# Kernel tuning notes

Measured on AMD Instinct MI355X. Metric: run time of the kernel, lower is better.

Reference implementation:

```python
import jax, jax.numpy as jnp
import numpy as np

B, N, F = 16, 1024, 256
HEADS, K, DOUT = 8, 512, 256
TAU = 1.0
EPS = 1e-08


def setup_inputs() -> dict:
    key = jax.random.key(0)
    k1, k2, k3, k4, k5, k6 = jax.random.split(key, 6)
    return {
        'Q': jax.random.normal(k1, (B, N, F), dtype=jnp.float32),
        'keys': jax.random.uniform(k2, (HEADS, K, F), dtype=jnp.float32),
        'conv_w': jax.random.normal(k3, (HEADS,), dtype=jnp.float32),
        'lin_w': jax.random.normal(k4, (DOUT, F), dtype=jnp.float32) * 0.05,
        'lin_b': jax.random.normal(k5, (DOUT,), dtype=jnp.float32) * 0.05,
        'mask': jax.random.randint(k6, (B, N), 0, 2, dtype=jnp.int32),
    }


def kl_reg(C):
    # C: (B, N, K)
    P = C ** 2
    cn = jnp.sum(C, axis=-2, keepdims=True) + EPS          # sum over N
    P = P / cn
    pn = jnp.sum(P, axis=-1, keepdims=True) + EPS          # sum over K
    P = P / pn
    kl = jnp.sum(P * (jnp.log(P + EPS) - jnp.log(C + EPS)))
    return 100.0 * kl


def memconv_fwd(Q, keys, conv_w, lin_w, lin_b, fmask):
    # pairwise L2 distance Q (B,N,F) vs keys (H,K,F) -> C (B,H,N,K)
    q2 = jnp.sum(Q * Q, axis=-1)                            # (B,N)
    k2 = jnp.sum(keys * keys, axis=-1)                      # (H,K)
    qk = jnp.einsum('bnf,hkf->bhnk', Q, keys)               # (B,H,N,K)
    d2 = q2[:, None, :, None] + k2[None, :, None, :] - 2.0 * qk
    C = jnp.sqrt(jnp.maximum(d2, 0.0))
    em = fmask[:, None, :, None]                            # (B,1,N,1) broadcast
    C = C * em
    # student-t kernel (gmn variant)
    C = (1.0 + C ** 2 / TAU) ** (-(0.5 * TAU + 0.5))
    C = C / jnp.sum(C, axis=-1, keepdims=True)
    C = C * em
    # conv1x1 over heads -> (B,N,K)
    C = jnp.einsum('bhnk,h->bnk', C, conv_w)
    C = jax.nn.softmax(C, axis=-1)
    C = C * fmask[:, :, None]
    kl = kl_reg(C)
    V = jnp.einsum('bnk,bnf->bkf', C, Q)                    # (B,K,F)
    out = jax.nn.leaky_relu(jnp.einsum('bkf,of->bko', V, lin_w) + lin_b, 0.01)
    return out, kl


def reference(Q, keys, conv_w, lin_w, lin_b, mask):
    fmask = mask.astype(Q.dtype)
    return memconv_fwd(Q, keys, conv_w, lin_w, lin_b, fmask)
```

## Files before the change

kernel.cpp:

```cpp
#include <hip/hip_runtime.h>
#include <math.h>

#define Bc 16
#define Nc 1024
#define Fc 256
#define Hc 8
#define Kc 512
#define DOUTc 256
#define EPSc 1e-8f

typedef short v8s __attribute__((ext_vector_type(8)));
typedef float v4f __attribute__((ext_vector_type(4)));

__device__ __forceinline__ float waveReduceSum(float v) {
    v += __shfl_xor(v, 32); v += __shfl_xor(v, 16); v += __shfl_xor(v, 8);
    v += __shfl_xor(v, 4);  v += __shfl_xor(v, 2);  v += __shfl_xor(v, 1);
    return v;
}

__device__ __forceinline__ unsigned short f2bf(float f) {
    unsigned int u = __float_as_uint(f);
    u = (u + 0x7fffu + ((u >> 16) & 1u)) >> 16;
    return (unsigned short)u;
}

__device__ __forceinline__ void lds_barrier() {
    __builtin_amdgcn_s_waitcnt(0xC07F);
    __builtin_amdgcn_s_barrier();
}

__global__ __launch_bounds__(256) void prep_all(
    const float* __restrict__ Q, const float* __restrict__ keys,
    const float* __restrict__ lin_w,
    float* __restrict__ k2g, unsigned short* __restrict__ Kp,
    unsigned short* __restrict__ Qbp, unsigned short* __restrict__ Wp,
    float* __restrict__ cn, float* __restrict__ klout) {
    __shared__ unsigned short T2[32][66];
    const int bx = blockIdx.x;
    const int tid = threadIdx.x;
    if (bx < 1024) {
        int row = bx * 4 + (tid >> 6);
        int l = tid & 63;
        float4 v = *(const float4*)(keys + (size_t)row * Fc + l * 4);
        float s = v.x * v.x + v.y * v.y + v.z * v.z + v.w * v.w;
        s = waveReduceSum(s);
        if (l == 0) k2g[row] = s;
    } else if (bx < 1536) {
        int t = (bx - 1024) * 256 + tid;
        int lane = t & 63, ci = t >> 6;
        int ct = ci & 7, ks = (ci >> 3) & 7, wv = (ci >> 6) & 3, h = ci >> 8;
        int qd = lane >> 4, li = lane & 15;
        int col = h * 512 + wv * 128 + ct * 16 + li;
        const float* src = keys + (size_t)col * Fc + ks * 32 + qd * 8;
        float4 a = *(const float4*)src;
        float4 b = *(const float4*)(src + 4);
        *(ushort4*)(Kp + (size_t)t * 8) = make_ushort4(f2bf(a.x), f2bf(a.y), f2bf(a.z), f2bf(a.w));
        *(ushort4*)(Kp + (size_t)t * 8 + 4) = make_ushort4(f2bf(b.x), f2bf(b.y), f2bf(b.z), f2bf(b.w));
    } else if (bx < 3584) {
        int i = bx - 1536;
        int n0 = (i & 31) * 32, f0 = ((i >> 5) & 3) * 64, bb = i >> 7;
        {
            int n_l = tid >> 3, f_l = (tid & 7) * 8;
            const float* src = Q + ((size_t)(bb * Nc + n0 + n_l)) * Fc + f0 + f_l;
            float4 a = *(const float4*)src;
            float4 b = *(const float4*)(src + 4);
            T2[n_l][f_l + 0] = f2bf(a.x); T2[n_l][f_l + 1] = f2bf(a.y);
            T2[n_l][f_l + 2] = f2bf(a.z); T2[n_l][f_l + 3] = f2bf(a.w);
            T2[n_l][f_l + 4] = f2bf(b.x); T2[n_l][f_l + 5] = f2bf(b.y);
            T2[n_l][f_l + 6] = f2bf(b.z); T2[n_l][f_l + 7] = f2bf(b.w);
        }
        __syncthreads();
        int c = tid >> 6, L = tid & 63;
        int qd = L >> 4, li = L & 15;
        unsigned short o[8];
#pragma unroll
        for (int j = 0; j < 8; j++) o[j] = T2[qd * 8 + j][c * 16 + li];
        size_t idx = ((((size_t)bb * 16 + (f0 >> 4) + c) * 32 + (n0 >> 5)) * 64 + L) * 8;
        *(ushort4*)(Qbp + idx) = make_ushort4(o[0], o[1], o[2], o[3]);
        *(ushort4*)(Qbp + idx + 4) = make_ushort4(o[4], o[5], o[6], o[7]);
    } else if (bx < 3616) {
        int t = (bx - 3584) * 256 + tid;
        int lane = t & 63, ci = t >> 6;
        int ot = ci >> 3, fs = ci & 7;
        int qd = lane >> 4, li = lane & 15;
        const float* src = lin_w + (size_t)(ot * 16 + li) * Fc + fs * 32 + qd * 8;
        float4 a = *(const float4*)src;
        float4 b = *(const float4*)(src + 4);
        *(ushort4*)(Wp + (size_t)t * 8) = make_ushort4(f2bf(a.x), f2bf(a.y), f2bf(a.z), f2bf(a.w));
        *(ushort4*)(Wp + (size_t)t * 8 + 4) = make_ushort4(f2bf(b.x), f2bf(b.y), f2bf(b.z), f2bf(b.w));
    } else {
        int i = (bx - 3616) * 256 + tid;
        float4 z = make_float4(0.f, 0.f, 0.f, 0.f);
        float4* d = (float4*)(cn + (size_t)i * 16);
        d[0] = z; d[1] = z; d[2] = z; d[3] = z;
        if (bx == 3616 && tid == 0) *klout = 0.f;
    }
}

__global__ __launch_bounds__(256, 2) void cmfma_kernel(
    const float* __restrict__ Q, const unsigned short* __restrict__ Kp,
    const float* __restrict__ k2g, const float* __restrict__ conv_w,
    const int* __restrict__ mask, float* __restrict__ C,
    float* __restrict__ cn, unsigned short* __restrict__ Ctp) {
    __shared__ __align__(16) char uni[36864];
    __shared__ float q2h[4][16];
    __shared__ float msh[32];
    __shared__ float redb[Hc][4][32];
    __shared__ float mslot[4][32];
    __shared__ float eslot[4][32];
    float* k2s = (float*)uni;
    short* Ash = (short*)(uni + 16384);
    short (*Tb)[36] = (short (*)[36])uni;

    const int tid = threadIdx.x;
    const int wv = tid >> 6, L = tid & 63;
    const int qd = L >> 4, li = L & 15;
    const int gr0 = blockIdx.x * 32;
    const int b = gr0 >> 10;

    {
        int s_ = wv >> 1;
        int ksbase = (wv & 1) * 4;
        const float* qrow = Q + (size_t)(gr0 + s_ * 16 + li) * Fc + qd * 8;
        float q2part = 0.f;
#pragma unroll
        for (int j = 0; j < 4; j++) {
            int ks = ksbase + j;
            float4 a = *(const float4*)(qrow + ks * 32);
            float4 bq = *(const float4*)(qrow + ks * 32 + 4);
            v8s f;
            f[0] = (short)f2bf(a.x);  f[1] = (short)f2bf(a.y);
            f[2] = (short)f2bf(a.z);  f[3] = (short)f2bf(a.w);
            f[4] = (short)f2bf(bq.x); f[5] = (short)f2bf(bq.y);
            f[6] = (short)f2bf(bq.z); f[7] = (short)f2bf(bq.w);
            *(v8s*)&Ash[(((s_ * 8 + ks) * 64) + L) * 8] = f;
            q2part += a.x * a.x + a.y * a.y + a.z * a.z + a.w * a.w +
                      bq.x * bq.x + bq.y * bq.y + bq.z * bq.z + bq.w * bq.w;
        }
        q2part += __shfl_xor(q2part, 16);
        q2part += __shfl_xor(q2part, 32);
        if (qd == 0) q2h[wv][li] = q2part;
    }
    if (tid < 32) msh[tid] = (float)mask[gr0 + tid];
    for (int i = tid; i < Hc * Kc / 4; i += 256)
        *(float4*)&k2s[i * 4] = *(const float4*)(k2g + i * 4);

    v4f D[2][8], S[2][8];
#pragma unroll
    for (int s = 0; s < 2; s++)
#pragma unroll
        for (int ct = 0; ct < 8; ct++) {
            D[s][ct] = (v4f){0.f, 0.f, 0.f, 0.f};
            S[s][ct] = (v4f){0.f, 0.f, 0.f, 0.f};
        }

    const unsigned short* kwbase = Kp + (size_t)L * 8;
    v8s Bc0[8], Bn[8];
    {
        const unsigned short* p0 = kwbase + (size_t)(wv * 64) * 512;
#pragma unroll
        for (int ct = 0; ct < 8; ct++) Bc0[ct] = *(const v8s*)(p0 + ct * 512);
    }

    lds_barrier();

    float q2r[2][4], mrow[2][4];
#pragma unroll
    for (int s = 0; s < 2; s++)
#pragma unroll
        for (int r = 0; r < 4; r++) {
            q2r[s][r] = q2h[2 * s][qd * 4 + r] + q2h[2 * s + 1][qd * 4 + r];
            mrow[s][r] = msh[s * 16 + qd * 4 + r];
        }

#define LD_A(s, kk) (*(const v8s*)&Ash[(((s) * 8 + (kk)) * 64 + L) * 8])

    v8s Ac0 = LD_A(0, 0);
    v8s Ac1 = LD_A(1, 0);

#define KSTEP(kk, CUR, NXT)                                                        \
    do {                                                                           \
        int hn = h * 8 + (kk) + 1;                                                 \
        int hh = (hn >> 3) & 7, kn = hn & 7;                                       \
        const unsigned short* pb =                                                 \
            kwbase + (size_t)(((hh * 4 + wv) * 64 + kn * 8)) * 512;                \
        _Pragma("unroll") for (int ct = 0; ct < 8; ct++)                           \
            NXT[ct] = *(const v8s*)(pb + ct * 512);                                \
        v8s An0 = LD_A(0, ((kk) + 1) & 7);                                         \
        v8s An1 = LD_A(1, ((kk) + 1) & 7);                                         \
        _Pragma("unroll") for (int ct = 0; ct < 8; ct++)                           \
            D[0][ct] = __builtin_amdgcn_mfma_f32_16x16x32_bf16(Ac0, CUR[ct],       \
                                                               D[0][ct], 0, 0, 0);\
        _Pragma("unroll") for (int ct = 0; ct < 8; ct++)                           \
            D[1][ct] = __builtin_amdgcn_mfma_f32_16x16x32_bf16(Ac1, CUR[ct],       \
                                                               D[1][ct], 0, 0, 0);\
        Ac0 = An0; Ac1 = An1;                                                      \
    } while (0)

    for (int h = 0; h < Hc; ++h) {
        KSTEP(0, Bc0, Bn); KSTEP(1, Bn, Bc0);
        KSTEP(2, Bc0, Bn); KSTEP(3, Bn, Bc0);
        KSTEP(4, Bc0, Bn); KSTEP(5, Bn, Bc0);
        KSTEP(6, Bc0, Bn); KSTEP(7, Bn, Bc0);

        float rs[2][4] = {{0.f, 0.f, 0.f, 0.f}, {0.f, 0.f, 0.f, 0.f}};
#pragma unroll
        for (int ct = 0; ct < 8; ct++) {
            float k2v = k2s[h * Kc + wv * 128 + ct * 16 + li];
#pragma unroll
            for (int s = 0; s < 2; s++)
#pragma unroll
                for (int r = 0; r < 4; r++) {
                    float d2 = fmaxf(q2r[s][r] + k2v - 2.f * D[s][ct][r], 0.f) * mrow[s][r];
                    float t = __builtin_amdgcn_rcpf(1.f + d2);
                    D[s][ct][r] = t;
                    rs[s][r] += t;
                }
        }
#pragma unroll
        for (int s = 0; s < 2; s++)
#pragma unroll
            for (int r = 0; r < 4; r++) {
                rs[s][r] += __shfl_xor(rs[s][r], 1, 16);
                rs[s][r] += __shfl_xor(rs[s][r], 2, 16);
                rs[s][r] += __shfl_xor(rs[s][r], 4, 16);
                rs[s][r] += __shfl_xor(rs[s][r], 8, 16);
            }
        if (li == 0) {
#pragma unroll
            for (int s = 0; s < 2; s++)
#pragma unroll
                for (int r = 0; r < 4; r++) redb[h][wv][s * 16 + qd * 4 + r] = rs[s][r];
        }
        lds_barrier();
        float wh = conv_w[h];
        float sc[2][4];
#pragma unroll
        for (int s = 0; s < 2; s++)
#pragma unroll
            for (int r = 0; r < 4; r++) {
                int rw = s * 16 + qd * 4 + r;
                float tot = redb[h][0][rw] + redb[h][1][rw] + redb[h][2][rw] + redb[h][3][rw];
                sc[s][r] = wh * __builtin_amdgcn_rcpf(tot);
            }
#pragma unroll
        for (int s = 0; s < 2; s++)
#pragma unroll
            for (int ct = 0; ct < 8; ct++)
#pragma unroll
                for (int r = 0; r < 4; r++) {
                    S[s][ct][r] += sc[s][r] * D[s][ct][r];
                    D[s][ct][r] = 0.f;
                }
    }
#undef KSTEP
#undef LD_A

    float mx[2][4] = {{-1e30f, -1e30f, -1e30f, -1e30f}, {-1e30f, -1e30f, -1e30f, -1e30f}};
#pragma unroll
    for (int s = 0; s < 2; s++)
#pragma unroll
        for (int ct = 0; ct < 8; ct++)
#pragma unroll
            for (int r = 0; r < 4; r++) mx[s][r] = fmaxf(mx[s][r], S[s][ct][r]);
#pragma unroll
    for (int s = 0; s < 2; s++)
#pragma unroll
        for (int r = 0; r < 4; r++) {
            mx[s][r] = fmaxf(mx[s][r], __shfl_xor(mx[s][r], 1, 16));
            mx[s][r] = fmaxf(mx[s][r], __shfl_xor(mx[s][r], 2, 16));
            mx[s][r] = fmaxf(mx[s][r], __shfl_xor(mx[s][r], 4, 16));
            mx[s][r] = fmaxf(mx[s][r], __shfl_xor(mx[s][r], 8, 16));
        }
    if (li == 0) {
#pragma unroll
        for (int s = 0; s < 2; s++)
#pragma unroll
            for (int r = 0; r < 4; r++) mslot[wv][s * 16 + qd * 4 + r] = mx[s][r];
    }
    lds_barrier();
#pragma unroll
    for (int s = 0; s < 2; s++)
#pragma unroll
        for (int r = 0; r < 4; r++) {
            int rw = s * 16 + qd * 4 + r;
            mx[s][r] = fmaxf(fmaxf(mslot[0][rw], mslot[1][rw]),
                             fmaxf(mslot[2][rw], mslot[3][rw]));
        }
    float es[2][4] = {{0.f, 0.f, 0.f, 0.f}, {0.f, 0.f, 0.f, 0.f}};
#pragma unroll
    for (int s = 0; s < 2; s++)
#pragma unroll
        for (int ct = 0; ct < 8; ct++)
#pragma unroll
            for (int r = 0; r < 4; r++) {
                float e = __expf(S[s][ct][r] - mx[s][r]);
                S[s][ct][r] = e;
                es[s][r] += e;
            }
#pragma unroll
    for (int s = 0; s < 2; s++)
#pragma unroll
        for (int r = 0; r < 4; r++) {
            es[s][r] += __shfl_xor(es[s][r], 1, 16);
            es[s][r] += __shfl_xor(es[s][r], 2, 16);
            es[s][r] += __shfl_xor(es[s][r], 4, 16);
            es[s][r] += __shfl_xor(es[s][r], 8, 16);
        }
    if (li == 0) {
#pragma unroll
        for (int s = 0; s < 2; s++)
#pragma unroll
            for (int r = 0; r < 4; r++) eslot[wv][s * 16 + qd * 4 + r] = es[s][r];
    }
    lds_barrier();
    float inv[2][4];
#pragma unroll
    for (int s = 0; s < 2; s++)
#pragma unroll
        for (int r = 0; r < 4; r++) {
            int rw = s * 16 + qd * 4 + r;
            float tot = eslot[0][rw] + eslot[1][rw] + eslot[2][rw] + eslot[3][rw];
            inv[s][r] = mrow[s][r] / tot;
        }
#pragma unroll
    for (int ct = 0; ct < 8; ct++) {
        int k = wv * 128 + ct * 16 + li;
        float colsum = 0.f;
#pragma unroll
        for (int s = 0; s < 2; s++) {
            float cv[4];
#pragma unroll
            for (int r = 0; r < 4; r++) {
                cv[r] = S[s][ct][r] * inv[s][r];
                C[(size_t)(gr0 + s * 16 + qd * 4 + r) * Kc + k] = cv[r];
                colsum += cv[r];
            }
            short4 t4;
            t4.x = (short)f2bf(cv[0]); t4.y = (short)f2bf(cv[1]);
            t4.z = (short)f2bf(cv[2]); t4.w = (short)f2bf(cv[3]);
            *(short4*)&Tb[k][s * 16 + qd * 4] = t4;
        }
        colsum += __shfl_xor(colsum, 16);
        colsum += __shfl_xor(colsum, 32);
        if (qd == 0) atomicAdd(&cn[b * Kc + k], colsum);
    }
    lds_barrier();
    {
        const int ns0 = (gr0 & 1023) >> 5;
#pragma unroll
        for (int kk = 0; kk < 2; kk++) {
            int k = tid * 2 + kk;
            int kt = k >> 4, klo = k & 15;
            size_t cbase = (((size_t)b * 32 + kt) * 32 + ns0) * 512;
#pragma unroll
            for (int q2i = 0; q2i < 4; q2i++) {
                short4 lo = *(short4*)&Tb[k][q2i * 8];
                short4 hi = *(short4*)&Tb[k][q2i * 8 + 4];
                short4* d = (short4*)(Ctp + cbase + (size_t)(q2i * 16 + klo) * 8);
                d[0] = lo; d[1] = hi;
            }
        }
    }
}

__global__ __launch_bounds__(256) void klv_kernel(
    const unsigned short* __restrict__ Ctp, const unsigned short* __restrict__ Qbp,
    unsigned short* __restrict__ Vp, const float* __restrict__ C,
    const float* __restrict__ cn, float* __restrict__ klout) {
    __shared__ short Vt[64][76];
    __shared__ float red[4];
    int tid = threadIdx.x;
    int bx = blockIdx.x;
    if (bx < 512) {
        int w = tid >> 6, L = tid & 63;
        int qd = L >> 4, li = L & 15;
        int wr = w >> 1, wc = w & 1;
        int bb = bx >> 5;
        int rem = bx & 31;
        int ktb = rem >> 2, ftb = rem & 3;
        int KT0 = ktb * 4 + wr * 2;
        int FT0 = ftb * 4 + wc * 2;
        const unsigned short* pa0 = Ctp + (((size_t)bb * 32 + KT0) * 32) * 512 + L * 8;
        const unsigned short* pa1 = pa0 + (size_t)32 * 512;
        const unsigned short* pb0 = Qbp + (((size_t)bb * 16 + FT0) * 32) * 512 + L * 8;
        const unsigned short* pb1 = pb0 + (size_t)32 * 512;
        v4f acc[2][2];
#pragma unroll
        for (int a = 0; a < 2; a++)
#pragma unroll
            for (int c = 0; c < 2; c++) acc[a][c] = (v4f){0.f, 0.f, 0.f, 0.f};

        v8s A0 = *(const v8s*)pa0, A1 = *(const v8s*)pa1;
        v8s B0 = *(const v8s*)pb0, B1 = *(const v8s*)pb1;
        for (int ns = 0; ns < 32; ns++) {
            int nsn = (ns + 1) & 31;
            v8s A0n = *(const v8s*)(pa0 + nsn * 512);
            v8s A1n = *(const v8s*)(pa1 + nsn * 512);
            v8s B0n = *(const v8s*)(pb0 + nsn * 512);
            v8s B1n = *(const v8s*)(pb1 + nsn * 512);
            acc[0][0] = __builtin_amdgcn_mfma_f32_16x16x32_bf16(A0, B0, acc[0][0], 0, 0, 0);
            acc[0][1] = __builtin_amdgcn_mfma_f32_16x16x32_bf16(A0, B1, acc[0][1], 0, 0, 0);
            acc[1][0] = __builtin_amdgcn_mfma_f32_16x16x32_bf16(A1, B0, acc[1][0], 0, 0, 0);
            acc[1][1] = __builtin_amdgcn_mfma_f32_16x16x32_bf16(A1, B1, acc[1][1], 0, 0, 0);
            A0 = A0n; A1 = A1n; B0 = B0n; B1 = B1n;
        }
#pragma unroll
        for (int a = 0; a < 2; a++)
#pragma unroll
            for (int c = 0; c < 2; c++)
#pragma unroll
                for (int r = 0; r < 4; r++)
                    Vt[(wr * 2 + a) * 16 + qd * 4 + r][(wc * 2 + c) * 16 + li] =
                        (short)f2bf(acc[a][c][r]);
        __syncthreads();
        {
            int ci = tid >> 5, s5 = tid & 31;
            int mtl = ci >> 1, fsl = ci & 1;
            size_t mt_g = (size_t)bb * 32 + ktb * 4 + mtl;
            size_t fs_g = (size_t)ftb * 2 + fsl;
#pragma unroll
            for (int half = 0; half < 2; half++) {
                int L2 = s5 + half * 32;
                int qd2 = L2 >> 4, li2 = L2 & 15;
                short4 x0 = *(short4*)&Vt[mtl * 16 + li2][fsl * 32 + qd2 * 8];
                short4 x1 = *(short4*)&Vt[mtl * 16 + li2][fsl * 32 + qd2 * 8 + 4];
                short4* d = (short4*)(Vp + ((mt_g * 8 + fs_g) * 64 + L2) * 8);
                d[0] = x0; d[1] = x1;
            }
        }
    } else {
        int bk = bx - 512;
        int w = tid >> 6, l = tid & 63;
        float kacc = 0.f;
#pragma unroll
        for (int rr = 0; rr < 4; rr++) {
            int row = bk * 16 + w * 4 + rr;
            int b = row >> 10;
            const float* cp = C + (size_t)row * Kc + l * 8;
            const float* np = cn + b * Kc + l * 8;
            float4 c0 = *(const float4*)cp;
            float4 c1 = *(const float4*)(cp + 4);
            float4 n0 = *(const float4*)np;
            float4 n1 = *(const float4*)(np + 4);
            float p[8];
            p[0] = c0.x * c0.x / (n0.x + EPSc); p[1] = c0.y * c0.y / (n0.y + EPSc);
            p[2] = c0.z * c0.z / (n0.z + EPSc); p[3] = c0.w * c0.w / (n0.w + EPSc);
            p[4] = c1.x * c1.x / (n1.x + EPSc); p[5] = c1.y * c1.y / (n1.y + EPSc);
            p[6] = c1.z * c1.z / (n1.z + EPSc); p[7] = c1.w * c1.w / (n1.w + EPSc);
            float s = p[0] + p[1] + p[2] + p[3] + p[4] + p[5] + p[6] + p[7];
            float pn = waveReduceSum(s) + EPSc;
            float rpn = 1.0f / pn;
            float cc[8] = {c0.x, c0.y, c0.z, c0.w, c1.x, c1.y, c1.z, c1.w};
#pragma unroll
            for (int j = 0; j < 8; j++) {
                float P = p[j] * rpn;
                kacc += P * __logf((P + EPSc) / (cc[j] + EPSc));
            }
        }
        kacc = waveReduceSum(kacc);
        if (l == 0) red[w] = kacc;
        __syncthreads();
        if (tid == 0)
            atomicAdd(klout, 100.f * (red[0] + red[1] + red[2] + red[3]));
    }
}

__global__ __launch_bounds__(256) void ofma_kernel(
    const unsigned short* __restrict__ Vp, const unsigned short* __restrict__ Wp,
    const float* __restrict__ bias, float* __restrict__ out) {
    int tid = threadIdx.x;
    int w = tid >> 6, L = tid & 63;
    int qd = L >> 4, li = L & 15;
    int wr = w >> 1, wc = w & 1;
    int MT0 = blockIdx.x * 4 + wr * 2;
    int OT0 = blockIdx.y * 4 + wc * 2;
    const unsigned short* pa0 = Vp + ((size_t)MT0 * 8) * 512 + L * 8;
    const unsigned short* pa1 = pa0 + (size_t)8 * 512;
    const unsigned short* pb0 = Wp + ((size_t)OT0 * 8) * 512 + L * 8;
    const unsigned short* pb1 = pb0 + (size_t)8 * 512;
    v4f acc[2][2];
#pragma unroll
    for (int a = 0; a < 2; a++)
#pragma unroll
        for (int c = 0; c < 2; c++) acc[a][c] = (v4f){0.f, 0.f, 0.f, 0.f};
#pragma unroll
    for (int fs = 0; fs < 8; fs++) {
        v8s A0 = *(const v8s*)(pa0 + fs * 512);
        v8s A1 = *(const v8s*)(pa1 + fs * 512);
        v8s B0 = *(const v8s*)(pb0 + fs * 512);
        v8s B1 = *(const v8s*)(pb1 + fs * 512);
        acc[0][0] = __builtin_amdgcn_mfma_f32_16x16x32_bf16(A0, B0, acc[0][0], 0, 0, 0);
        acc[0][1] = __builtin_amdgcn_mfma_f32_16x16x32_bf16(A0, B1, acc[0][1], 0, 0, 0);
        acc[1][0] = __builtin_amdgcn_mfma_f32_16x16x32_bf16(A1, B0, acc[1][0], 0, 0, 0);
        acc[1][1] = __builtin_amdgcn_mfma_f32_16x16x32_bf16(A1, B1, acc[1][1], 0, 0, 0);
    }
#pragma unroll
    for (int c = 0; c < 2; c++) {
        float bv = bias[(OT0 + c) * 16 + li];
#pragma unroll
        for (int a = 0; a < 2; a++)
#pragma unroll
            for (int r = 0; r < 4; r++) {
                int m = (MT0 + a) * 16 + qd * 4 + r;
                int o = (OT0 + c) * 16 + li;
                float x = acc[a][c][r] + bv;
                out[(size_t)m * DOUTc + o] = x > 0.f ? x : 0.01f * x;
            }
    }
}

extern "C" void kernel_launch(void* const* d_in, const int* in_sizes, int n_in,
                              void* d_out, int out_size, void* d_ws, size_t ws_size,
                              hipStream_t stream) {
    const float* Q = (const float*)d_in[0];
    const float* keys = (const float*)d_in[1];
    const float* conv_w = (const float*)d_in[2];
    const float* lin_w = (const float*)d_in[3];
    const float* lin_b = (const float*)d_in[4];
    const int* mask = (const int*)d_in[5];

    float* out = (float*)d_out;
    float* kl = out + (size_t)Bc * Kc * DOUTc;

    float* ws = (float*)d_ws;
    float* C = ws;
    float* k2 = C + (size_t)Bc * Nc * Kc;
    float* cn = k2 + (size_t)Hc * Kc;
    unsigned short* Kp = (unsigned short*)(cn + (size_t)Bc * Kc);
    unsigned short* Ctp = Kp + (size_t)Hc * Kc * Fc;
    unsigned short* Qbp = Ctp + (size_t)Bc * Nc * Kc;
    unsigned short* Vp = Qbp + (size_t)Bc * Nc * Fc;
    unsigned short* Wp = Vp + (size_t)Bc * Kc * Fc;

    prep_all<<<3618, 256, 0, stream>>>(Q, keys, lin_w, k2, Kp, Qbp, Wp, cn, kl);
    cmfma_kernel<<<Bc * Nc / 32, 256, 0, stream>>>(Q, Kp, k2, conv_w, mask, C, cn, Ctp);
    klv_kernel<<<1536, 256, 0, stream>>>(Ctp, Qbp, Vp, C, cn, kl);
    ofma_kernel<<<dim3(Bc * Kc / 64, DOUTc / 64), 256, 0, stream>>>(Vp, Wp, lin_b, out);
}
```

Before: 165.7 us.

## Prefetch MFMA operands two steps ahead, fold +1 into k2, raise MFMA priority

Several small tweaks land together. Two GEMM loops now double-buffer their operands so the loads for steps ns+2 and ns+3 are issued while the current MFMAs run. The distance kernel folds the +1 into the k2 table, which turns the student-t denominator into a single fma plus max, and drops the per-element mask multiply. That is safe only because masked rows are zeroed again later. The MFMA bursts are wrapped in s_setprio, the KL pass hoists per-column reciprocals and uses fast rcp in place of divisions, and the k2 prep uses fewer blocks that each loop over rows.

```diff
diff --git a/kernel.cpp b/kernel.cpp
--- a/kernel.cpp
+++ b/kernel.cpp
@@ -38,15 +38,18 @@
     __shared__ unsigned short T2[32][66];
     const int bx = blockIdx.x;
     const int tid = threadIdx.x;
-    if (bx < 1024) {
-        int row = bx * 4 + (tid >> 6);
-        int l = tid & 63;
-        float4 v = *(const float4*)(keys + (size_t)row * Fc + l * 4);
-        float s = v.x * v.x + v.y * v.y + v.z * v.z + v.w * v.w;
-        s = waveReduceSum(s);
-        if (l == 0) k2g[row] = s;
-    } else if (bx < 1536) {
-        int t = (bx - 1024) * 256 + tid;
+    if (bx < 64) {
+        int wv = tid >> 6, l = tid & 63;
+#pragma unroll 4
+        for (int rr = 0; rr < 16; rr++) {
+            int row = bx * 64 + wv * 16 + rr;
+            float4 v = *(const float4*)(keys + (size_t)row * Fc + l * 4);
+            float s = v.x * v.x + v.y * v.y + v.z * v.z + v.w * v.w;
+            s = waveReduceSum(s);
+            if (l == 0) k2g[row] = s + 1.0f;
+        }
+    } else if (bx < 576) {
+        int t = (bx - 64) * 256 + tid;
         int lane = t & 63, ci = t >> 6;
         int ct = ci & 7, ks = (ci >> 3) & 7, wv = (ci >> 6) & 3, h = ci >> 8;
         int qd = lane >> 4, li = lane & 15;
@@ -56,8 +59,8 @@
         float4 b = *(const float4*)(src + 4);
         *(ushort4*)(Kp + (size_t)t * 8) = make_ushort4(f2bf(a.x), f2bf(a.y), f2bf(a.z), f2bf(a.w));
         *(ushort4*)(Kp + (size_t)t * 8 + 4) = make_ushort4(f2bf(b.x), f2bf(b.y), f2bf(b.z), f2bf(b.w));
-    } else if (bx < 3584) {
-        int i = bx - 1536;
+    } else if (bx < 2624) {
+        int i = bx - 576;
         int n0 = (i & 31) * 32, f0 = ((i >> 5) & 3) * 64, bb = i >> 7;
         {
             int n_l = tid >> 3, f_l = (tid & 7) * 8;
@@ -78,8 +81,8 @@
         size_t idx = ((((size_t)bb * 16 + (f0 >> 4) + c) * 32 + (n0 >> 5)) * 64 + L) * 8;
         *(ushort4*)(Qbp + idx) = make_ushort4(o[0], o[1], o[2], o[3]);
         *(ushort4*)(Qbp + idx + 4) = make_ushort4(o[4], o[5], o[6], o[7]);
-    } else if (bx < 3616) {
-        int t = (bx - 3584) * 256 + tid;
+    } else if (bx < 2656) {
+        int t = (bx - 2624) * 256 + tid;
         int lane = t & 63, ci = t >> 6;
         int ot = ci >> 3, fs = ci & 7;
         int qd = lane >> 4, li = lane & 15;
@@ -89,11 +92,11 @@
         *(ushort4*)(Wp + (size_t)t * 8) = make_ushort4(f2bf(a.x), f2bf(a.y), f2bf(a.z), f2bf(a.w));
         *(ushort4*)(Wp + (size_t)t * 8 + 4) = make_ushort4(f2bf(b.x), f2bf(b.y), f2bf(b.z), f2bf(b.w));
     } else {
-        int i = (bx - 3616) * 256 + tid;
+        int i = (bx - 2656) * 256 + tid;
         float4 z = make_float4(0.f, 0.f, 0.f, 0.f);
         float4* d = (float4*)(cn + (size_t)i * 16);
         d[0] = z; d[1] = z; d[2] = z; d[3] = z;
-        if (bx == 3616 && tid == 0) *klout = 0.f;
+        if (bx == 2656 && tid == 0) *klout = 0.f;
     }
 }
 
@@ -188,12 +191,14 @@
             NXT[ct] = *(const v8s*)(pb + ct * 512);                                \
         v8s An0 = LD_A(0, ((kk) + 1) & 7);                                         \
         v8s An1 = LD_A(1, ((kk) + 1) & 7);                                         \
+        __builtin_amdgcn_s_setprio(1);                                             \
         _Pragma("unroll") for (int ct = 0; ct < 8; ct++)                           \
             D[0][ct] = __builtin_amdgcn_mfma_f32_16x16x32_bf16(Ac0, CUR[ct],       \
                                                                D[0][ct], 0, 0, 0);\
         _Pragma("unroll") for (int ct = 0; ct < 8; ct++)                           \
             D[1][ct] = __builtin_amdgcn_mfma_f32_16x16x32_bf16(Ac1, CUR[ct],       \
                                                                D[1][ct], 0, 0, 0);\
+        __builtin_amdgcn_s_setprio(0);                                             \
         Ac0 = An0; Ac1 = An1;                                                      \
     } while (0)
 
@@ -211,8 +216,8 @@
             for (int s = 0; s < 2; s++)
 #pragma unroll
                 for (int r = 0; r < 4; r++) {
-                    float d2 = fmaxf(q2r[s][r] + k2v - 2.f * D[s][ct][r], 0.f) * mrow[s][r];
-                    float t = __builtin_amdgcn_rcpf(1.f + d2);
+                    float x = fmaf(-2.f, D[s][ct][r], q2r[s][r] + k2v);
+                    float t = __builtin_amdgcn_rcpf(fmaxf(x, 1.0f));
                     D[s][ct][r] = t;
                     rs[s][r] += t;
                 }
@@ -391,19 +396,25 @@
 #pragma unroll
             for (int c = 0; c < 2; c++) acc[a][c] = (v4f){0.f, 0.f, 0.f, 0.f};
 
-        v8s A0 = *(const v8s*)pa0, A1 = *(const v8s*)pa1;
-        v8s B0 = *(const v8s*)pb0, B1 = *(const v8s*)pb1;
-        for (int ns = 0; ns < 32; ns++) {
-            int nsn = (ns + 1) & 31;
-            v8s A0n = *(const v8s*)(pa0 + nsn * 512);
-            v8s A1n = *(const v8s*)(pa1 + nsn * 512);
-            v8s B0n = *(const v8s*)(pb0 + nsn * 512);
-            v8s B1n = *(const v8s*)(pb1 + nsn * 512);
-            acc[0][0] = __builtin_amdgcn_mfma_f32_16x16x32_bf16(A0, B0, acc[0][0], 0, 0, 0);
-            acc[0][1] = __builtin_amdgcn_mfma_f32_16x16x32_bf16(A0, B1, acc[0][1], 0, 0, 0);
-            acc[1][0] = __builtin_amdgcn_mfma_f32_16x16x32_bf16(A1, B0, acc[1][0], 0, 0, 0);
-            acc[1][1] = __builtin_amdgcn_mfma_f32_16x16x32_bf16(A1, B1, acc[1][1], 0, 0, 0);
-            A0 = A0n; A1 = A1n; B0 = B0n; B1 = B1n;
+        v8s Ae0 = *(const v8s*)pa0, Ae1 = *(const v8s*)pa1;
+        v8s Be0 = *(const v8s*)pb0, Be1 = *(const v8s*)pb1;
+        v8s Ao0 = *(const v8s*)(pa0 + 512), Ao1 = *(const v8s*)(pa1 + 512);
+        v8s Bo0 = *(const v8s*)(pb0 + 512), Bo1 = *(const v8s*)(pb1 + 512);
+        for (int ns = 0; ns < 32; ns += 2) {
+            int n2 = (ns + 2) & 31;
+            int n3 = (ns + 3) & 31;
+            acc[0][0] = __builtin_amdgcn_mfma_f32_16x16x32_bf16(Ae0, Be0, acc[0][0], 0, 0, 0);
+            acc[0][1] = __builtin_amdgcn_mfma_f32_16x16x32_bf16(Ae0, Be1, acc[0][1], 0, 0, 0);
+            acc[1][0] = __builtin_amdgcn_mfma_f32_16x16x32_bf16(Ae1, Be0, acc[1][0], 0, 0, 0);
+            acc[1][1] = __builtin_amdgcn_mfma_f32_16x16x32_bf16(Ae1, Be1, acc[1][1], 0, 0, 0);
+            Ae0 = *(const v8s*)(pa0 + n2 * 512); Ae1 = *(const v8s*)(pa1 + n2 * 512);
+            Be0 = *(const v8s*)(pb0 + n2 * 512); Be1 = *(const v8s*)(pb1 + n2 * 512);
+            acc[0][0] = __builtin_amdgcn_mfma_f32_16x16x32_bf16(Ao0, Bo0, acc[0][0], 0, 0, 0);
+            acc[0][1] = __builtin_amdgcn_mfma_f32_16x16x32_bf16(Ao0, Bo1, acc[0][1], 0, 0, 0);
+            acc[1][0] = __builtin_amdgcn_mfma_f32_16x16x32_bf16(Ao1, Bo0, acc[1][0], 0, 0, 0);
+            acc[1][1] = __builtin_amdgcn_mfma_f32_16x16x32_bf16(Ao1, Bo1, acc[1][1], 0, 0, 0);
+            Ao0 = *(const v8s*)(pa0 + n3 * 512); Ao1 = *(const v8s*)(pa1 + n3 * 512);
+            Bo0 = *(const v8s*)(pb0 + n3 * 512); Bo1 = *(const v8s*)(pb1 + n3 * 512);
         }
 #pragma unroll
         for (int a = 0; a < 2; a++)
@@ -432,30 +443,34 @@
     } else {
         int bk = bx - 512;
         int w = tid >> 6, l = tid & 63;
+        int b0 = (bk * 16) >> 10;
+        const float* np = cn + b0 * Kc + l * 8;
+        v4f n0 = *(const v4f*)np;
+        v4f n1 = *(const v4f*)(np + 4);
+        float rn[8];
+#pragma unroll
+        for (int j = 0; j < 4; j++) {
+            rn[j] = __builtin_amdgcn_rcpf(n0[j] + EPSc);
+            rn[4 + j] = __builtin_amdgcn_rcpf(n1[j] + EPSc);
+        }
         float kacc = 0.f;
 #pragma unroll
         for (int rr = 0; rr < 4; rr++) {
             int row = bk * 16 + w * 4 + rr;
-            int b = row >> 10;
             const float* cp = C + (size_t)row * Kc + l * 8;
-            const float* np = cn + b * Kc + l * 8;
-            float4 c0 = *(const float4*)cp;
-            float4 c1 = *(const float4*)(cp + 4);
-            float4 n0 = *(const float4*)np;
-            float4 n1 = *(const float4*)(np + 4);
+            v4f c0 = *(const v4f*)cp;
+            v4f c1 = *(const v4f*)(cp + 4);
+            float cc[8] = {c0[0], c0[1], c0[2], c0[3], c1[0], c1[1], c1[2], c1[3]};
             float p[8];
-            p[0] = c0.x * c0.x / (n0.x + EPSc); p[1] = c0.y * c0.y / (n0.y + EPSc);
-            p[2] = c0.z * c0.z / (n0.z + EPSc); p[3] = c0.w * c0.w / (n0.w + EPSc);
-            p[4] = c1.x * c1.x / (n1.x + EPSc); p[5] = c1.y * c1.y / (n1.y + EPSc);
-            p[6] = c1.z * c1.z / (n1.z + EPSc); p[7] = c1.w * c1.w / (n1.w + EPSc);
+#pragma unroll
+            for (int j = 0; j < 8; j++) p[j] = cc[j] * cc[j] * rn[j];
             float s = p[0] + p[1] + p[2] + p[3] + p[4] + p[5] + p[6] + p[7];
             float pn = waveReduceSum(s) + EPSc;
-            float rpn = 1.0f / pn;
-            float cc[8] = {c0.x, c0.y, c0.z, c0.w, c1.x, c1.y, c1.z, c1.w};
+            float rpn = __builtin_amdgcn_rcpf(pn);
 #pragma unroll
             for (int j = 0; j < 8; j++) {
                 float P = p[j] * rpn;
-                kacc += P * __logf((P + EPSc) / (cc[j] + EPSc));
+                kacc += P * __logf((P + EPSc) * __builtin_amdgcn_rcpf(cc[j] + EPSc));
             }
         }
         kacc = waveReduceSum(kacc);
@@ -484,16 +499,26 @@
     for (int a = 0; a < 2; a++)
 #pragma unroll
         for (int c = 0; c < 2; c++) acc[a][c] = (v4f){0.f, 0.f, 0.f, 0.f};
-#pragma unroll
-    for (int fs = 0; fs < 8; fs++) {
-        v8s A0 = *(const v8s*)(pa0 + fs * 512);
-        v8s A1 = *(const v8s*)(pa1 + fs * 512);
-        v8s B0 = *(const v8s*)(pb0 + fs * 512);
-        v8s B1 = *(const v8s*)(pb1 + fs * 512);
-        acc[0][0] = __builtin_amdgcn_mfma_f32_16x16x32_bf16(A0, B0, acc[0][0], 0, 0, 0);
-        acc[0][1] = __builtin_amdgcn_mfma_f32_16x16x32_bf16(A0, B1, acc[0][1], 0, 0, 0);
-        acc[1][0] = __builtin_amdgcn_mfma_f32_16x16x32_bf16(A1, B0, acc[1][0], 0, 0, 0);
-        acc[1][1] = __builtin_amdgcn_mfma_f32_16x16x32_bf16(A1, B1, acc[1][1], 0, 0, 0);
+    v8s Ae0 = *(const v8s*)pa0, Ae1 = *(const v8s*)pa1;
+    v8s Be0 = *(const v8s*)pb0, Be1 = *(const v8s*)pb1;
+    v8s Ao0 = *(const v8s*)(pa0 + 512), Ao1 = *(const v8s*)(pa1 + 512);
+    v8s Bo0 = *(const v8s*)(pb0 + 512), Bo1 = *(const v8s*)(pb1 + 512);
+#pragma unroll
+    for (int fs = 0; fs < 8; fs += 2) {
+        int n2 = (fs + 2) & 7;
+        int n3 = (fs + 3) & 7;
+        acc[0][0] = __builtin_amdgcn_mfma_f32_16x16x32_bf16(Ae0, Be0, acc[0][0], 0, 0, 0);
+        acc[0][1] = __builtin_amdgcn_mfma_f32_16x16x32_bf16(Ae0, Be1, acc[0][1], 0, 0, 0);
+        acc[1][0] = __builtin_amdgcn_mfma_f32_16x16x32_bf16(Ae1, Be0, acc[1][0], 0, 0, 0);
+        acc[1][1] = __builtin_amdgcn_mfma_f32_16x16x32_bf16(Ae1, Be1, acc[1][1], 0, 0, 0);
+        Ae0 = *(const v8s*)(pa0 + n2 * 512); Ae1 = *(const v8s*)(pa1 + n2 * 512);
+        Be0 = *(const v8s*)(pb0 + n2 * 512); Be1 = *(const v8s*)(pb1 + n2 * 512);
+        acc[0][0] = __builtin_amdgcn_mfma_f32_16x16x32_bf16(Ao0, Bo0, acc[0][0], 0, 0, 0);
+        acc[0][1] = __builtin_amdgcn_mfma_f32_16x16x32_bf16(Ao0, Bo1, acc[0][1], 0, 0, 0);
+        acc[1][0] = __builtin_amdgcn_mfma_f32_16x16x32_bf16(Ao1, Bo0, acc[1][0], 0, 0, 0);
+        acc[1][1] = __builtin_amdgcn_mfma_f32_16x16x32_bf16(Ao1, Bo1, acc[1][1], 0, 0, 0);
+        Ao0 = *(const v8s*)(pa0 + n3 * 512); Ao1 = *(const v8s*)(pa1 + n3 * 512);
+        Bo0 = *(const v8s*)(pb0 + n3 * 512); Bo1 = *(const v8s*)(pb1 + n3 * 512);
     }
 #pragma unroll
     for (int c = 0; c < 2; c++) {
@@ -533,7 +558,7 @@
     unsigned short* Vp = Qbp + (size_t)Bc * Nc * Fc;
     unsigned short* Wp = Vp + (size_t)Bc * Kc * Fc;
 
-    prep_all<<<3618, 256, 0, stream>>>(Q, keys, lin_w, k2, Kp, Qbp, Wp, cn, kl);
+    prep_all<<<2658, 256, 0, stream>>>(Q, keys, lin_w, k2, Kp, Qbp, Wp, cn, kl);
     cmfma_kernel<<<Bc * Nc / 32, 256, 0, stream>>>(Q, Kp, k2, conv_w, mask, C, cn, Ctp);
     klv_kernel<<<1536, 256, 0, stream>>>(Ctp, Qbp, Vp, C, cn, kl);
     ofma_kernel<<<dim3(Bc * Kc / 64, DOUTc / 64), 256, 0, stream>>>(Vp, Wp, lin_b, out);
```

After: 172.2 us. 3.9% more time.
